# Kernel optimization log

Measured on AMD Instinct MI355X. Metric: run time of the kernel, lower is better.

Reference implementation:

```python
import jax, jax.numpy as jnp
import numpy as np

B, T, E = 2, 2048, 1024
H, D = 16, 64          # num_heads, head_dim (v_head_dim == head_dim)


def setup_inputs() -> dict:
    key = jax.random.key(0)
    ks = jax.random.split(key, 10)
    s = lambda fan_in: 1.0 / np.sqrt(fan_in)
    inp = {
        "embed": jax.random.normal(ks[0], (B, T, E), dtype=jnp.float32),
        "mask": jax.random.randint(ks[1], (B, T, T), 0, 2) > 0,
        # Linear weights stored as [in, out] (y = x @ W + b)
        "Wq": jax.random.uniform(ks[2], (E, H * D), minval=-s(E), maxval=s(E)),
        "bq": jnp.zeros((H * D,), jnp.float32),
        "Wk": jax.random.uniform(ks[3], (E, H * D), minval=-s(E), maxval=s(E)),
        "bk": jnp.zeros((H * D,), jnp.float32),
        "Wv": jax.random.uniform(ks[4], (E, H * D), minval=-s(E), maxval=s(E)),
        "bv": jnp.zeros((H * D,), jnp.float32),
        "Wz": jax.random.uniform(ks[5], (H * D, E), minval=-s(H * D), maxval=s(H * D)),
        "bz": jnp.zeros((E,), jnp.float32),
    }
    return inp


def reference(embed, mask, Wq, bq, Wk, bk, Wv, bv, Wz, bz):
    # Self-attention: context = embed
    q = (embed @ Wq + bq).reshape(B, T, H, D)   # b t h d
    k = (embed @ Wk + bk).reshape(B, T, H, D)   # b T h d
    v = (embed @ Wv + bv).reshape(B, T, H, D)   # b T h d

    scale = D ** (-0.5)
    score = jnp.einsum('bthd,bThd->bhtT', q, k) * scale   # [b,h,t,T] materialized, as in source
    max_neg = -jnp.finfo(score.dtype).max
    score = jnp.where(mask[:, None, :, :], score, max_neg)
    norm_score = jax.nn.softmax(score, axis=-1)
    z = jnp.einsum('bhtT,bThd->bthd', norm_score, v)      # [b,t,h,d]
    flat_z = z.reshape(B, T, H * D)
    return flat_z @ Wz + bz
```

## Files before the change

kernel.cpp:

```cpp
#include <hip/hip_runtime.h>
#include <hip/hip_bf16.h>


typedef __bf16 bf8_t  __attribute__((ext_vector_type(8)));
typedef __bf16 bf4_t  __attribute__((ext_vector_type(4)));
typedef float  f4_t   __attribute__((ext_vector_type(4)));

constexpr int Bb = 2, Tt = 2048, Hh = 16, Dd = 64;

#define ASYNC16(g, l)                                                        \
    __builtin_amdgcn_global_load_lds(                                        \
        (const __attribute__((address_space(1))) void*)(g),                  \
        (__attribute__((address_space(3))) void*)(l), 16, 0, 0)

#if __has_builtin(__builtin_amdgcn_exp2f)
#define EXP2F(x) __builtin_amdgcn_exp2f(x)
#else
#define EXP2F(x) exp2f(x)
#endif

__global__ __launch_bounds__(256) void convert_kernel(
    const float* __restrict__ in, __bf16* __restrict__ out)
{
    int i = (blockIdx.x * 256 + threadIdx.x) * 4;
    float4 v = *reinterpret_cast<const float4*>(in + i);
    bf4_t o = {(__bf16)v.x, (__bf16)v.y, (__bf16)v.z, (__bf16)v.w};
    *reinterpret_cast<bf4_t*>(out + i) = o;
}

__global__ __launch_bounds__(256) void maskbias_kernel(
    const int* __restrict__ m, __bf16* __restrict__ o)
{
    int i = (blockIdx.x * 256 + threadIdx.x) * 4;
    int4 v = *reinterpret_cast<const int4*>(m + i);
    const __bf16 z = (__bf16)0.f, neg = (__bf16)(-1e30f);
    bf4_t r = {v.x ? z : neg, v.y ? z : neg, v.z ? z : neg, v.w ? z : neg};
    *reinterpret_cast<bf4_t*>(o + i) = r;
}

__global__ __launch_bounds__(256) void transpose_kernel(
    const float* __restrict__ w0, const float* __restrict__ w1,
    const float* __restrict__ w2, const float* __restrict__ w3,
    __bf16* __restrict__ o0, __bf16* __restrict__ o1,
    __bf16* __restrict__ o2, __bf16* __restrict__ o3)
{
    const float* in; __bf16* out;
    switch (blockIdx.z) {
        case 0: in = w0; out = o0; break;
        case 1: in = w1; out = o1; break;
        case 2: in = w2; out = o2; break;
        default: in = w3; out = o3; break;
    }
    __shared__ float t[32][33];
    int x  = threadIdx.x & 31;
    int y0 = threadIdx.x >> 5;
    int bx = blockIdx.x * 32;
    int by = blockIdx.y * 32;
    #pragma unroll
    for (int i = 0; i < 4; i++) {
        int y = y0 + i * 8;
        t[y][x] = in[(size_t)(by + y) * 1024 + bx + x];
    }
    __syncthreads();
    #pragma unroll
    for (int i = 0; i < 4; i++) {
        int y = y0 + i * 8;
        out[(size_t)(bx + y) * 1024 + by + x] = (__bf16)t[x][y];
    }
}

template <int TM, typename OutT>
__device__ __forceinline__ void gemm_body(const __bf16* __restrict__ A,
                                          const __bf16* __restrict__ Bt,
                                          const float* __restrict__ bias,
                                          OutT* __restrict__ out,
                                          int mode, float oscale, int bx, int by)
{
    constexpr int NI = TM / 32;
    alignas(16) __shared__ __bf16 As[TM * 64];
    alignas(16) __shared__ __bf16 Bs[128 * 64];

    int tid  = threadIdx.x;
    int lane = tid & 63;
    int quad = lane >> 4;
    int l16  = lane & 15;
    int wave = tid >> 6;
    int wm   = wave >> 1, wn = wave & 1;

    f4_t acc[NI][4];
    #pragma unroll
    for (int i = 0; i < NI; i++)
        #pragma unroll
        for (int j = 0; j < 4; j++)
            acc[i][j] = f4_t{0.f, 0.f, 0.f, 0.f};

    for (int kt = 0; kt < 1024; kt += 64) {
        #pragma unroll
        for (int i = 0; i < TM / 32; i++) {
            int c   = tid + 256 * i;
            int row = c >> 3, j = c & 7;
            ASYNC16(A + (size_t)(by * TM + row) * 1024 + kt + ((j ^ (row & 7)) * 8),
                    &As[c * 8]);
        }
        #pragma unroll
        for (int i = 0; i < 4; i++) {
            int c   = tid + 256 * i;
            int row = c >> 3, j = c & 7;
            ASYNC16(Bt + (size_t)(bx * 128 + row) * 1024 + kt + ((j ^ (row & 7)) * 8),
                    &Bs[c * 8]);
        }
        __syncthreads();

        bf8_t af[2][NI], bfr[2][4];
        #pragma unroll
        for (int c = 0; c < 2; c++) {
            #pragma unroll
            for (int im = 0; im < NI; im++) {
                int row = wm * (TM / 2) + im * 16 + l16;
                af[c][im] = *reinterpret_cast<const bf8_t*>(
                    &As[row * 64 + (((c * 4 + quad) ^ (row & 7)) * 8)]);
            }
            #pragma unroll
            for (int in_ = 0; in_ < 4; in_++) {
                int row = wn * 64 + in_ * 16 + l16;
                bfr[c][in_] = *reinterpret_cast<const bf8_t*>(
                    &Bs[row * 64 + (((c * 4 + quad) ^ (row & 7)) * 8)]);
            }
        }
        #pragma unroll
        for (int c = 0; c < 2; c++)
            #pragma unroll
            for (int im = 0; im < NI; im++)
                #pragma unroll
                for (int in_ = 0; in_ < 4; in_++)
                    acc[im][in_] = __builtin_amdgcn_mfma_f32_16x16x32_bf16(
                        af[c][im], bfr[c][in_], acc[im][in_], 0, 0, 0);
        __syncthreads();
    }

    #pragma unroll
    for (int im = 0; im < NI; im++) {
        #pragma unroll
        for (int in_ = 0; in_ < 4; in_++) {
            int gc  = bx * 128 + wn * 64 + in_ * 16 + l16;
            float bb = bias[gc];
            int gr0 = by * TM + wm * (TM / 2) + im * 16 + quad * 4;
            #pragma unroll
            for (int r = 0; r < 4; r++) {
                int gr  = gr0 + r;
                float v = (acc[im][in_][r] + bb) * oscale;
                size_t idx;
                if (mode == 0) {
                    idx = (size_t)gr * 1024 + gc;
                } else {
                    int b = gr >> 11, t = gr & 2047;
                    int h = gc >> 6,  d = gc & 63;
                    if (mode == 1) idx = ((size_t)(b * Hh + h) * Tt + t) * Dd + d;
                    else           idx = ((size_t)(b * Hh + h) * Dd + d) * Tt + t;
                }
                out[idx] = (OutT)v;
            }
        }
    }
}

__global__ __launch_bounds__(256) void gemm_qkv_kernel(
    const __bf16* __restrict__ A,
    const __bf16* __restrict__ WqT, const __bf16* __restrict__ WkT, const __bf16* __restrict__ WvT,
    const float* __restrict__ bq,  const float* __restrict__ bk,  const float* __restrict__ bv,
    __bf16* __restrict__ Qo, __bf16* __restrict__ Ko, __bf16* __restrict__ Vo)
{
    const __bf16* Bt; const float* bias; __bf16* out; int mode; float sc;
    if      (blockIdx.z == 0) { Bt = WqT; bias = bq; out = Qo; mode = 1; sc = 0.18033688011112042f; }
    else if (blockIdx.z == 1) { Bt = WkT; bias = bk; out = Ko; mode = 1; sc = 1.f; }
    else                      { Bt = WvT; bias = bv; out = Vo; mode = 2; sc = 1.f; }
    gemm_body<128, __bf16>(A, Bt, bias, out, mode, sc, blockIdx.x, blockIdx.y);
}

__global__ __launch_bounds__(256) void gemm_out_kernel(
    const __bf16* __restrict__ A, const __bf16* __restrict__ Bt,
    const float* __restrict__ bias, float* __restrict__ out)
{
    gemm_body<64, float>(A, Bt, bias, out, 0, 1.f, blockIdx.x, blockIdx.y);
}

__global__ __launch_bounds__(512, 4) void flash_kernel(
    const __bf16* __restrict__ Qb, const __bf16* __restrict__ Kb,
    const __bf16* __restrict__ Vb, const __bf16* __restrict__ biasb,
    __bf16* __restrict__ Zb)
{
    alignas(16) __shared__ char smem[25600];
    __bf16* Ks = (__bf16*)smem;
    __bf16* Vs = (__bf16*)(smem + 8192);
    __bf16* Ps = (__bf16*)(smem + 16384);

    int tid  = threadIdx.x;
    int lane = tid & 63;
    int wave = tid >> 6;
    int quad = lane >> 4;
    int l16  = lane & 15;
    int g    = wave >> 2;
    int qw   = wave & 3;
    int b = blockIdx.z, h = blockIdx.y;
    int bh = b * Hh + h;
    int qrow = blockIdx.x * 64 + qw * 16;

    int srow = tid >> 3, sj = tid & 7;
    const __bf16* kgp = Kb + ((size_t)bh * Tt + srow) * Dd + ((sj ^ (srow & 7)) * 8);
    const __bf16* vgp = Vb + ((size_t)bh * Dd + srow) * Tt + ((sj ^ (srow & 7)) * 8);

    bf8_t qf[2];
    #pragma unroll
    for (int c = 0; c < 2; c++)
        qf[c] = *reinterpret_cast<const bf8_t*>(
            Qb + ((size_t)bh * Tt + qrow + l16) * Dd + c * 32 + quad * 8);

    const __bf16* bp = biasb + ((size_t)b * Tt + qrow + l16) * Tt + g * 32 + quad * 4;

    float l_i = 0.f;
    f4_t o[4];
    #pragma unroll
    for (int d = 0; d < 4; d++) o[d] = f4_t{0.f, 0.f, 0.f, 0.f};

    __bf16* pw = Ps + wave * 16 * 36;

    for (int kt = 0; kt < Tt; kt += 64) {
        ASYNC16(kgp + (size_t)kt * Dd, &Ks[tid * 8]);
        ASYNC16(vgp + kt,              &Vs[tid * 8]);
        __syncthreads();

        f4_t s[2];
        #pragma unroll
        for (int n = 0; n < 2; n++) {
            bf4_t bv = *reinterpret_cast<const bf4_t*>(bp + kt + n * 16);
            s[n] = f4_t{(float)bv[0], (float)bv[1], (float)bv[2], (float)bv[3]};
        }
        #pragma unroll
        for (int c = 0; c < 2; c++)
            #pragma unroll
            for (int n = 0; n < 2; n++) {
                int krow = g * 32 + n * 16 + l16;
                bf8_t kf = *reinterpret_cast<const bf8_t*>(
                    &Ks[krow * 64 + (((c * 4 + quad) ^ (krow & 7)) * 8)]);
                s[n] = __builtin_amdgcn_mfma_f32_16x16x32_bf16(kf, qf[c], s[n], 0, 0, 0);
            }

        float rs = 0.f;
        #pragma unroll
        for (int n = 0; n < 2; n++) {
            bf4_t pv4;
            #pragma unroll
            for (int r = 0; r < 4; r++) {
                float p = EXP2F(s[n][r]);
                rs += p;
                pv4[r] = (__bf16)p;
            }
            *reinterpret_cast<bf4_t*>(&pw[l16 * 36 + n * 16 + quad * 4]) = pv4;
        }
        rs += __shfl_xor(rs, 16);
        rs += __shfl_xor(rs, 32);
        l_i += rs;

        bf8_t pf = *reinterpret_cast<const bf8_t*>(&pw[l16 * 36 + quad * 8]);
        #pragma unroll
        for (int ds = 0; ds < 4; ds++) {
            int vrow = ds * 16 + l16;
            bf8_t vf = *reinterpret_cast<const bf8_t*>(
                &Vs[vrow * 64 + (((g * 4 + quad) ^ (vrow & 7)) * 8)]);
            o[ds] = __builtin_amdgcn_mfma_f32_16x16x32_bf16(vf, pf, o[ds], 0, 0, 0);
        }
        __syncthreads();
    }

    float* Os = (float*)smem;
    float* Ls = (float*)(smem + 17408);
    if (g == 0) {
        #pragma unroll
        for (int ds = 0; ds < 4; ds++)
            *reinterpret_cast<f4_t*>(&Os[(qw * 16 + l16) * 68 + ds * 16 + quad * 4]) = o[ds];
        Ls[qw * 16 + l16] = l_i;
    }
    __syncthreads();
    if (g == 1) {
        float inv = 1.f / fmaxf(Ls[qw * 16 + l16] + l_i, 1e-30f);
        size_t zrow = ((size_t)b * Tt + qrow + l16) * 1024 + h * 64;
        #pragma unroll
        for (int ds = 0; ds < 4; ds++) {
            f4_t o0 = *reinterpret_cast<const f4_t*>(
                &Os[(qw * 16 + l16) * 68 + ds * 16 + quad * 4]);
            bf4_t ov;
            #pragma unroll
            for (int r = 0; r < 4; r++) ov[r] = (__bf16)((o0[r] + o[ds][r]) * inv);
            *reinterpret_cast<bf4_t*>(Zb + zrow + ds * 16 + quad * 4) = ov;
        }
    }
}

extern "C" void kernel_launch(void* const* d_in, const int* in_sizes, int n_in,
                              void* d_out, int out_size, void* d_ws, size_t ws_size,
                              hipStream_t stream)
{
    (void)in_sizes; (void)n_in; (void)out_size; (void)ws_size;

    const float* embed = (const float*)d_in[0];
    const int*   mask  = (const int*)d_in[1];
    const float* Wq = (const float*)d_in[2];
    const float* bq = (const float*)d_in[3];
    const float* Wk = (const float*)d_in[4];
    const float* bk = (const float*)d_in[5];
    const float* Wv = (const float*)d_in[6];
    const float* bv = (const float*)d_in[7];
    const float* Wz = (const float*)d_in[8];
    const float* bz = (const float*)d_in[9];
    float* out = (float*)d_out;

    char* ws = (char*)d_ws;
    const size_t MB = (size_t)1024 * 1024;
    __bf16* WqT = (__bf16*)(ws + 0 * MB);
    __bf16* WkT = (__bf16*)(ws + 2 * MB);
    __bf16* WvT = (__bf16*)(ws + 4 * MB);
    __bf16* WzT = (__bf16*)(ws + 6 * MB);
    __bf16* Eb  = (__bf16*)(ws + 8 * MB);
    __bf16* Qb  = (__bf16*)(ws + 16 * MB);
    __bf16* Kb  = (__bf16*)(ws + 24 * MB);
    __bf16* Vb  = (__bf16*)(ws + 32 * MB);
    __bf16* Zb  = (__bf16*)(ws + 40 * MB);
    __bf16* Mb  = (__bf16*)(ws + 48 * MB);

    convert_kernel<<<dim3(4096), 256, 0, stream>>>(embed, Eb);
    maskbias_kernel<<<dim3(8192), 256, 0, stream>>>(mask, Mb);
    transpose_kernel<<<dim3(32, 32, 4), 256, 0, stream>>>(Wq, Wk, Wv, Wz,
                                                          WqT, WkT, WvT, WzT);
    gemm_qkv_kernel<<<dim3(8, 32, 3), 256, 0, stream>>>(Eb, WqT, WkT, WvT,
                                                        bq, bk, bv, Qb, Kb, Vb);
    flash_kernel<<<dim3(32, Hh, Bb), 512, 0, stream>>>(Qb, Kb, Vb, Mb, Zb);
    gemm_out_kernel<<<dim3(8, 64, 1), 256, 0, stream>>>(Zb, WzT, bz, out);
}
```

Measured before the change: 251.5 us.

## Restructure flash kernel: 128-query blocks, register-prefetched double-buffered K/V

Each block now covers 128 query rows, with every wave handling 16 rows over the full 64-key tile, instead of splitting the keys between two wave groups. This removes the cross-group reduction of O and l through shared memory at the end. K, V and mask-bias tiles for the next iteration are prefetched into registers and stored into alternating LDS buffers, which drops the async global-to-LDS loads and the second barrier per iteration. The cost is a grid half as large (512 blocks), more registers per thread, and more LDS for the two buffers.

```diff
diff --git a/kernel.cpp b/kernel.cpp
--- a/kernel.cpp
+++ b/kernel.cpp
@@ -189,25 +189,23 @@
     const __bf16* __restrict__ Vb, const __bf16* __restrict__ biasb,
     __bf16* __restrict__ Zb)
 {
-    alignas(16) __shared__ char smem[25600];
-    __bf16* Ks = (__bf16*)smem;
-    __bf16* Vs = (__bf16*)(smem + 8192);
-    __bf16* Ps = (__bf16*)(smem + 16384);
+    alignas(16) __shared__ __bf16 Ks[2][64 * 64];
+    alignas(16) __shared__ __bf16 Vs[2][64 * 64];
+    alignas(16) __shared__ __bf16 Ps[8 * 16 * 72];
 
     int tid  = threadIdx.x;
     int lane = tid & 63;
     int wave = tid >> 6;
     int quad = lane >> 4;
     int l16  = lane & 15;
-    int g    = wave >> 2;
-    int qw   = wave & 3;
     int b = blockIdx.z, h = blockIdx.y;
     int bh = b * Hh + h;
-    int qrow = blockIdx.x * 64 + qw * 16;
+    int qrow = blockIdx.x * 128 + wave * 16;
 
     int srow = tid >> 3, sj = tid & 7;
     const __bf16* kgp = Kb + ((size_t)bh * Tt + srow) * Dd + ((sj ^ (srow & 7)) * 8);
     const __bf16* vgp = Vb + ((size_t)bh * Dd + srow) * Tt + ((sj ^ (srow & 7)) * 8);
+    const int sdst = tid * 8;
 
     bf8_t qf[2];
     #pragma unroll
@@ -215,39 +213,53 @@
         qf[c] = *reinterpret_cast<const bf8_t*>(
             Qb + ((size_t)bh * Tt + qrow + l16) * Dd + c * 32 + quad * 8);
 
-    const __bf16* bp = biasb + ((size_t)b * Tt + qrow + l16) * Tt + g * 32 + quad * 4;
+    const __bf16* bp = biasb + ((size_t)b * Tt + qrow + l16) * Tt + quad * 4;
 
     float l_i = 0.f;
     f4_t o[4];
     #pragma unroll
     for (int d = 0; d < 4; d++) o[d] = f4_t{0.f, 0.f, 0.f, 0.f};
 
-    __bf16* pw = Ps + wave * 16 * 36;
+    __bf16* pw = Ps + wave * 16 * 72;
+
+    bf8_t kreg = *reinterpret_cast<const bf8_t*>(kgp);
+    bf8_t vreg = *reinterpret_cast<const bf8_t*>(vgp);
+    bf4_t breg[4];
+    #pragma unroll
+    for (int n = 0; n < 4; n++)
+        breg[n] = *reinterpret_cast<const bf4_t*>(bp + n * 16);
 
     for (int kt = 0; kt < Tt; kt += 64) {
-        ASYNC16(kgp + (size_t)kt * Dd, &Ks[tid * 8]);
-        ASYNC16(vgp + kt,              &Vs[tid * 8]);
+        int par = (kt >> 6) & 1;
+        *reinterpret_cast<bf8_t*>(&Ks[par][sdst]) = kreg;
+        *reinterpret_cast<bf8_t*>(&Vs[par][sdst]) = vreg;
+        f4_t s[4];
+        #pragma unroll
+        for (int n = 0; n < 4; n++)
+            s[n] = f4_t{(float)breg[n][0], (float)breg[n][1],
+                        (float)breg[n][2], (float)breg[n][3]};
         __syncthreads();
 
-        f4_t s[2];
-        #pragma unroll
-        for (int n = 0; n < 2; n++) {
-            bf4_t bv = *reinterpret_cast<const bf4_t*>(bp + kt + n * 16);
-            s[n] = f4_t{(float)bv[0], (float)bv[1], (float)bv[2], (float)bv[3]};
-        }
+        int ktn = (kt + 64 < Tt) ? kt + 64 : 0;
+        kreg = *reinterpret_cast<const bf8_t*>(kgp + (size_t)ktn * Dd);
+        vreg = *reinterpret_cast<const bf8_t*>(vgp + ktn);
+        #pragma unroll
+        for (int n = 0; n < 4; n++)
+            breg[n] = *reinterpret_cast<const bf4_t*>(bp + ktn + n * 16);
+
         #pragma unroll
         for (int c = 0; c < 2; c++)
             #pragma unroll
-            for (int n = 0; n < 2; n++) {
-                int krow = g * 32 + n * 16 + l16;
+            for (int n = 0; n < 4; n++) {
+                int krow = n * 16 + l16;
                 bf8_t kf = *reinterpret_cast<const bf8_t*>(
-                    &Ks[krow * 64 + (((c * 4 + quad) ^ (krow & 7)) * 8)]);
+                    &Ks[par][krow * 64 + (((c * 4 + quad) ^ (krow & 7)) * 8)]);
                 s[n] = __builtin_amdgcn_mfma_f32_16x16x32_bf16(kf, qf[c], s[n], 0, 0, 0);
             }
 
         float rs = 0.f;
         #pragma unroll
-        for (int n = 0; n < 2; n++) {
+        for (int n = 0; n < 4; n++) {
             bf4_t pv4;
             #pragma unroll
             for (int r = 0; r < 4; r++) {
@@ -255,44 +267,34 @@
                 rs += p;
                 pv4[r] = (__bf16)p;
             }
-            *reinterpret_cast<bf4_t*>(&pw[l16 * 36 + n * 16 + quad * 4]) = pv4;
+            *reinterpret_cast<bf4_t*>(&pw[l16 * 72 + n * 16 + quad * 4]) = pv4;
         }
         rs += __shfl_xor(rs, 16);
         rs += __shfl_xor(rs, 32);
         l_i += rs;
 
-        bf8_t pf = *reinterpret_cast<const bf8_t*>(&pw[l16 * 36 + quad * 8]);
-        #pragma unroll
-        for (int ds = 0; ds < 4; ds++) {
-            int vrow = ds * 16 + l16;
-            bf8_t vf = *reinterpret_cast<const bf8_t*>(
-                &Vs[vrow * 64 + (((g * 4 + quad) ^ (vrow & 7)) * 8)]);
-            o[ds] = __builtin_amdgcn_mfma_f32_16x16x32_bf16(vf, pf, o[ds], 0, 0, 0);
-        }
-        __syncthreads();
-    }
-
-    float* Os = (float*)smem;
-    float* Ls = (float*)(smem + 17408);
-    if (g == 0) {
-        #pragma unroll
-        for (int ds = 0; ds < 4; ds++)
-            *reinterpret_cast<f4_t*>(&Os[(qw * 16 + l16) * 68 + ds * 16 + quad * 4]) = o[ds];
-        Ls[qw * 16 + l16] = l_i;
-    }
-    __syncthreads();
-    if (g == 1) {
-        float inv = 1.f / fmaxf(Ls[qw * 16 + l16] + l_i, 1e-30f);
-        size_t zrow = ((size_t)b * Tt + qrow + l16) * 1024 + h * 64;
-        #pragma unroll
-        for (int ds = 0; ds < 4; ds++) {
-            f4_t o0 = *reinterpret_cast<const f4_t*>(
-                &Os[(qw * 16 + l16) * 68 + ds * 16 + quad * 4]);
-            bf4_t ov;
-            #pragma unroll
-            for (int r = 0; r < 4; r++) ov[r] = (__bf16)((o0[r] + o[ds][r]) * inv);
-            *reinterpret_cast<bf4_t*>(Zb + zrow + ds * 16 + quad * 4) = ov;
-        }
+        #pragma unroll
+        for (int c = 0; c < 2; c++) {
+            bf8_t pf = *reinterpret_cast<const bf8_t*>(
+                &pw[l16 * 72 + c * 32 + quad * 8]);
+            #pragma unroll
+            for (int ds = 0; ds < 4; ds++) {
+                int vrow = ds * 16 + l16;
+                bf8_t vf = *reinterpret_cast<const bf8_t*>(
+                    &Vs[par][vrow * 64 + (((c * 4 + quad) ^ (vrow & 7)) * 8)]);
+                o[ds] = __builtin_amdgcn_mfma_f32_16x16x32_bf16(vf, pf, o[ds], 0, 0, 0);
+            }
+        }
+    }
+
+    float inv = 1.f / fmaxf(l_i, 1e-30f);
+    size_t zrow = ((size_t)b * Tt + qrow + l16) * 1024 + h * 64;
+    #pragma unroll
+    for (int ds = 0; ds < 4; ds++) {
+        bf4_t ov;
+        #pragma unroll
+        for (int r = 0; r < 4; r++) ov[r] = (__bf16)(o[ds][r] * inv);
+        *reinterpret_cast<bf4_t*>(Zb + zrow + ds * 16 + quad * 4) = ov;
     }
 }
 
@@ -333,6 +335,6 @@
                                                           WqT, WkT, WvT, WzT);
     gemm_qkv_kernel<<<dim3(8, 32, 3), 256, 0, stream>>>(Eb, WqT, WkT, WvT,
                                                         bq, bk, bv, Qb, Kb, Vb);
-    flash_kernel<<<dim3(32, Hh, Bb), 512, 0, stream>>>(Qb, Kb, Vb, Mb, Zb);
+    flash_kernel<<<dim3(16, Hh, Bb), 512, 0, stream>>>(Qb, Kb, Vb, Mb, Zb);
     gemm_out_kernel<<<dim3(8, 64, 1), 256, 0, stream>>>(Zb, WzT, bz, out);
 }
```

Result: faster. 244.0 us (-3.0%).
